# Kernel optimization log

Measured on AMD Instinct MI355X. Metric: run time of the kernel, lower is better.

## Reference

```python
import jax, jax.numpy as jnp
import numpy as np

N_NODES = 40000
N_EDGES = 640000
IN_DIM = 128
HID = 128
N_GRAPHS = 256
N_CLASSES = 1


def setup_inputs() -> dict:
    key = jax.random.key(0)
    ks = jax.random.split(key, 16)
    h = jax.random.normal(ks[0], (N_NODES, IN_DIM), dtype=jnp.float32)
    src = jax.random.randint(ks[1], (N_EDGES,), 0, N_NODES, dtype=jnp.int32)
    dst = jax.random.randint(ks[2], (N_EDGES,), 0, N_NODES, dtype=jnp.int32)
    graph_ids = jnp.sort(jax.random.randint(ks[3], (N_NODES,), 0, N_GRAPHS, dtype=jnp.int32))
    s = 1.0 / np.sqrt(HID)
    W1 = jax.random.normal(ks[4], (IN_DIM, HID), dtype=jnp.float32) * s
    b1 = jnp.zeros((HID,), jnp.float32)
    W2 = jax.random.normal(ks[5], (HID, HID), dtype=jnp.float32) * s
    b2 = jnp.zeros((HID,), jnp.float32)
    Wc1 = jax.random.normal(ks[6], (HID, HID), dtype=jnp.float32) * s
    bc1 = jnp.zeros((HID,), jnp.float32)
    Wc2 = jax.random.normal(ks[7], (HID, HID), dtype=jnp.float32) * s
    bc2 = jnp.zeros((HID,), jnp.float32)
    Wc3 = jax.random.normal(ks[8], (HID, N_CLASSES), dtype=jnp.float32) * s
    bc3 = jnp.zeros((N_CLASSES,), jnp.float32)
    return dict(h=h, src=src, dst=dst, graph_ids=graph_ids,
                W1=W1, b1=b1, W2=W2, b2=b2,
                Wc1=Wc1, bc1=bc1, Wc2=Wc2, bc2=bc2, Wc3=Wc3, bc3=bc3)


def _graph_conv(h, src, dst, W, b):
    # DGL GraphConv with norm='both': out = D_in^{-1/2} A D_out^{-1/2} h W + b
    ones = jnp.ones((src.shape[0],), h.dtype)
    deg_out = jax.ops.segment_sum(ones, src, num_segments=N_NODES)
    deg_in = jax.ops.segment_sum(ones, dst, num_segments=N_NODES)
    norm_s = jnp.clip(deg_out, 1.0, None) ** -0.5  # [N]
    norm_d = jnp.clip(deg_in, 1.0, None) ** -0.5
    # mult weight first (in_dim >= out_dim path in DGL); math identical either way
    hw = (h * norm_s[:, None]) @ W                  # [N, HID]
    agg = jax.ops.segment_sum(hw[src], dst, num_segments=N_NODES)  # gather-scatter
    return agg * norm_d[:, None] + b


def reference(h, src, dst, graph_ids, W1, b1, W2, b2, Wc1, bc1, Wc2, bc2, Wc3, bc3):
    h1 = jax.nn.relu(_graph_conv(h, src, dst, W1, b1))
    h1 = jax.nn.relu(_graph_conv(h1, src, dst, W2, b2))
    # dgl.mean_nodes: per-graph mean over nodes
    sums = jax.ops.segment_sum(h1, graph_ids, num_segments=N_GRAPHS)      # [G, HID]
    counts = jax.ops.segment_sum(jnp.ones((N_NODES,), h1.dtype), graph_ids,
                                 num_segments=N_GRAPHS)
    hg = sums / jnp.maximum(counts, 1.0)[:, None]
    out = jax.nn.relu(hg @ Wc1 + bc1)
    out = jax.nn.relu(out @ Wc2 + bc2)
    return out @ Wc3 + bc3
```

## Files before the change

kernel.cpp:

```cpp
#include <hip/hip_runtime.h>

#define HID 128
#define CAP 64
#define HBLK 160
#define PERIOD 21

typedef unsigned int uint;
typedef unsigned short ushort;

typedef __attribute__((ext_vector_type(8))) short short8;
typedef __attribute__((ext_vector_type(4))) float floatx4;

static __device__ __forceinline__ ushort f2bf(float f) {
    uint u = __float_as_uint(f);
    u += 0x7fffu + ((u >> 16) & 1u);
    return (ushort)(u >> 16);
}
static __device__ __forceinline__ float bf2f(ushort v) {
    return __uint_as_float(((uint)v) << 16);
}

__global__ void gc_wpack(const float* __restrict__ W1, const float* __restrict__ W2,
                         uint4* __restrict__ wpk) {
    int which = blockIdx.x;
    const float* W = which ? W2 : W1;
    uint4* o = wpk + (size_t)which * 2048;
    for (int i = threadIdx.x; i < 2048; i += 256) {
        int lane = i & 63;
        int kc = (i >> 6) & 3;
        int nt = i >> 8;
        int n = nt * 16 + (lane & 15);
        int k0 = kc * 32 + (lane >> 4) * 8;
        uint p[4];
        #pragma unroll
        for (int j = 0; j < 4; ++j) {
            ushort a = f2bf(W[(size_t)(k0 + 2 * j) * HID + n]);
            ushort b = f2bf(W[(size_t)(k0 + 2 * j + 1) * HID + n]);
            p[j] = (uint)a | ((uint)b << 16);
        }
        uint4 v; v.x = p[0]; v.y = p[1]; v.z = p[2]; v.w = p[3];
        o[i] = v;
    }
}

__global__ void gc_build_mm(const int* __restrict__ src, const int* __restrict__ dst,
                            int* __restrict__ cnt_in, ushort* __restrict__ slot,
                            uint* __restrict__ pblock,
                            const float* __restrict__ X, const uint4* __restrict__ wpk,
                            ushort* __restrict__ hw, int n_edges, int n_nodes) {
    __shared__ uint hb4[10000];
    int b = blockIdx.x;
    int r = b % PERIOD, q = b / PERIOD;
    int t = threadIdx.x;

    if (r < 16) {
        int bi = q * 16 + r;
        if (bi >= 2500) return;
        int e = bi * 256 + t;
        if (e < n_edges) {
            int s = src[e], d = dst[e];
            int pos = atomicAdd(&cnt_in[d], 1);
            if (pos < CAP) slot[(size_t)d * CAP + pos] = (ushort)s;
        }
    } else if (r == 16) {
        int hq = q;
        if (hq >= HBLK) return;
        for (int i = t; i < 10000; i += 256) hb4[i] = 0u;
        __syncthreads();
        int per = (n_edges + HBLK - 1) / HBLK;
        int e0 = hq * per, e1 = min(e0 + per, n_edges);
        for (int e = e0 + t; e < e1; e += 256) {
            int s = src[e];
            atomicAdd(&hb4[s >> 2], 1u << ((s & 3) * 8));
        }
        __syncthreads();
        uint* o = pblock + (size_t)hq * 10000;
        for (int i = t; i < 10000; i += 256) o[i] = hb4[i];
    } else {
        int mb = q * 4 + (r - 17);
        if (mb >= 625) return;
        int wave = (mb * 256 + t) >> 6;
        int lane = t & 63;
        int tiles = n_nodes >> 4;
        if (wave >= tiles) return;
        int m = lane & 15, quad = lane >> 4;
        int node = wave * 16 + m;
        const float* xrow = X + (size_t)node * HID;

        floatx4 acc[8];
        #pragma unroll
        for (int nt = 0; nt < 8; ++nt) acc[nt] = (floatx4){0.f, 0.f, 0.f, 0.f};

        #pragma unroll
        for (int kc = 0; kc < 4; ++kc) {
            const float4 xa = *reinterpret_cast<const float4*>(xrow + kc * 32 + quad * 8);
            const float4 xb = *reinterpret_cast<const float4*>(xrow + kc * 32 + quad * 8 + 4);
            uint4 xu;
            xu.x = (uint)f2bf(xa.x) | ((uint)f2bf(xa.y) << 16);
            xu.y = (uint)f2bf(xa.z) | ((uint)f2bf(xa.w) << 16);
            xu.z = (uint)f2bf(xb.x) | ((uint)f2bf(xb.y) << 16);
            xu.w = (uint)f2bf(xb.z) | ((uint)f2bf(xb.w) << 16);
            short8 xf = *reinterpret_cast<short8*>(&xu);
            #pragma unroll
            for (int nt = 0; nt < 8; ++nt) {
                uint4 wu = wpk[(size_t)(nt * 4 + kc) * 64 + lane];
                short8 wf = *reinterpret_cast<short8*>(&wu);
                acc[nt] = __builtin_amdgcn_mfma_f32_16x16x32_bf16(wf, xf, acc[nt], 0, 0, 0);
            }
        }
        #pragma unroll
        for (int nt = 0; nt < 8; ++nt) {
            uint2 v;
            v.x = (uint)f2bf(acc[nt][0]) | ((uint)f2bf(acc[nt][1]) << 16);
            v.y = (uint)f2bf(acc[nt][2]) | ((uint)f2bf(acc[nt][3]) << 16);
            *reinterpret_cast<uint2*>(hw + (size_t)node * HID + nt * 16 + quad * 4) = v;
        }
    }
}

__global__ void gc_reduce(const uint* __restrict__ pblock, float* __restrict__ norm_s,
                          int n_nodes) {
    int i = blockIdx.x * blockDim.x + threadIdx.x;
    if (i >= 10000) return;
    uint a0 = 0, a1 = 0, a2 = 0, a3 = 0;
    for (int b = 0; b < HBLK; ++b) {
        uint v = pblock[(size_t)b * 10000 + i];
        a0 += v & 0xffu;
        a1 += (v >> 8) & 0xffu;
        a2 += (v >> 16) & 0xffu;
        a3 += v >> 24;
    }
    float4 o;
    o.x = rsqrtf(fmaxf((float)a0, 1.0f));
    o.y = rsqrtf(fmaxf((float)a1, 1.0f));
    o.z = rsqrtf(fmaxf((float)a2, 1.0f));
    o.w = rsqrtf(fmaxf((float)a3, 1.0f));
    *reinterpret_cast<float4*>(norm_s + i * 4) = o;
}

__global__ void gc_gather_mm(const ushort* __restrict__ HW, const int* __restrict__ cnt_in,
                             const float* __restrict__ norm_s, const ushort* __restrict__ slot,
                             const float* __restrict__ b, const uint4* __restrict__ wpk2,
                             ushort* __restrict__ hw2, int n_nodes) {
    __shared__ ushort tile[16 * HID];
    int tid = threadIdx.x;
    int ts = tid >> 4;
    int l16 = tid & 15;
    int node = blockIdx.x * 16 + ts;
    int q = l16 << 3;

    int ci = cnt_in[node];
    int cnt = min(ci, CAP);
    const ushort* row = slot + (size_t)node * CAP;
    float a[8];
    #pragma unroll
    for (int j = 0; j < 8; ++j) a[j] = 0.0f;

    auto accum = [&](uint4 u, float ns) {
        a[0] = fmaf(ns, __uint_as_float(u.x << 16), a[0]);
        a[1] = fmaf(ns, __uint_as_float(u.x & 0xffff0000u), a[1]);
        a[2] = fmaf(ns, __uint_as_float(u.y << 16), a[2]);
        a[3] = fmaf(ns, __uint_as_float(u.y & 0xffff0000u), a[3]);
        a[4] = fmaf(ns, __uint_as_float(u.z << 16), a[4]);
        a[5] = fmaf(ns, __uint_as_float(u.z & 0xffff0000u), a[5]);
        a[6] = fmaf(ns, __uint_as_float(u.w << 16), a[6]);
        a[7] = fmaf(ns, __uint_as_float(u.w & 0xffff0000u), a[7]);
    };

    int e = 0;
    for (; e + 3 < cnt; e += 4) {
        int s0 = row[e], s1 = row[e + 1], s2 = row[e + 2], s3 = row[e + 3];
        uint4 u0 = *reinterpret_cast<const uint4*>(HW + (size_t)s0 * HID + q);
        uint4 u1 = *reinterpret_cast<const uint4*>(HW + (size_t)s1 * HID + q);
        uint4 u2 = *reinterpret_cast<const uint4*>(HW + (size_t)s2 * HID + q);
        uint4 u3 = *reinterpret_cast<const uint4*>(HW + (size_t)s3 * HID + q);
        float n0 = norm_s[s0], n1 = norm_s[s1], n2 = norm_s[s2], n3 = norm_s[s3];
        accum(u0, n0); accum(u1, n1); accum(u2, n2); accum(u3, n3);
    }
    for (; e < cnt; ++e) {
        int s0 = row[e];
        uint4 u0 = *reinterpret_cast<const uint4*>(HW + (size_t)s0 * HID + q);
        accum(u0, norm_s[s0]);
    }

    float nd = rsqrtf(fmaxf((float)ci, 1.0f));
    const float4 bv0 = *reinterpret_cast<const float4*>(b + q);
    const float4 bv1 = *reinterpret_cast<const float4*>(b + q + 4);
    float r[8];
    r[0] = fmaxf(a[0] * nd + bv0.x, 0.0f);
    r[1] = fmaxf(a[1] * nd + bv0.y, 0.0f);
    r[2] = fmaxf(a[2] * nd + bv0.z, 0.0f);
    r[3] = fmaxf(a[3] * nd + bv0.w, 0.0f);
    r[4] = fmaxf(a[4] * nd + bv1.x, 0.0f);
    r[5] = fmaxf(a[5] * nd + bv1.y, 0.0f);
    r[6] = fmaxf(a[6] * nd + bv1.z, 0.0f);
    r[7] = fmaxf(a[7] * nd + bv1.w, 0.0f);
    uint4 v;
    v.x = (uint)f2bf(r[0]) | ((uint)f2bf(r[1]) << 16);
    v.y = (uint)f2bf(r[2]) | ((uint)f2bf(r[3]) << 16);
    v.z = (uint)f2bf(r[4]) | ((uint)f2bf(r[5]) << 16);
    v.w = (uint)f2bf(r[6]) | ((uint)f2bf(r[7]) << 16);
    *reinterpret_cast<uint4*>(&tile[ts * HID + ((l16 ^ ts) << 3)]) = v;
    __syncthreads();

    int wv = tid >> 6;
    int lane = tid & 63;
    int m = lane & 15, quad = lane >> 4;
    int onode = blockIdx.x * 16 + m;

    floatx4 acc0 = (floatx4){0.f, 0.f, 0.f, 0.f};
    floatx4 acc1 = (floatx4){0.f, 0.f, 0.f, 0.f};
    int nt0 = wv * 2, nt1 = wv * 2 + 1;
    #pragma unroll
    for (int kc = 0; kc < 4; ++kc) {
        int cc = (kc * 4 + quad) ^ m;
        uint4 xu = *reinterpret_cast<const uint4*>(&tile[m * HID + (cc << 3)]);
        short8 xf = *reinterpret_cast<short8*>(&xu);
        uint4 w0 = wpk2[(size_t)(nt0 * 4 + kc) * 64 + lane];
        uint4 w1 = wpk2[(size_t)(nt1 * 4 + kc) * 64 + lane];
        short8 wf0 = *reinterpret_cast<short8*>(&w0);
        short8 wf1 = *reinterpret_cast<short8*>(&w1);
        acc0 = __builtin_amdgcn_mfma_f32_16x16x32_bf16(wf0, xf, acc0, 0, 0, 0);
        acc1 = __builtin_amdgcn_mfma_f32_16x16x32_bf16(wf1, xf, acc1, 0, 0, 0);
    }
    float ns = norm_s[onode];
    {
        uint2 o0, o1;
        o0.x = (uint)f2bf(acc0[0] * ns) | ((uint)f2bf(acc0[1] * ns) << 16);
        o0.y = (uint)f2bf(acc0[2] * ns) | ((uint)f2bf(acc0[3] * ns) << 16);
        o1.x = (uint)f2bf(acc1[0] * ns) | ((uint)f2bf(acc1[1] * ns) << 16);
        o1.y = (uint)f2bf(acc1[2] * ns) | ((uint)f2bf(acc1[3] * ns) << 16);
        *reinterpret_cast<uint2*>(hw2 + (size_t)onode * HID + nt0 * 16 + quad * 4) = o0;
        *reinterpret_cast<uint2*>(hw2 + (size_t)onode * HID + nt1 * 16 + quad * 4) = o1;
    }
}

__global__ void gc_gather_pool(const ushort* __restrict__ HW, const int* __restrict__ cnt_in,
                               const ushort* __restrict__ slot, const int* __restrict__ gid,
                               const float* __restrict__ b, float* __restrict__ part2,
                               int n_nodes) {
    __shared__ float tile[16 * HID];
    __shared__ int sgid[16];
    int tid = threadIdx.x;
    int ts = tid >> 4;
    int l16 = tid & 15;
    int node = blockIdx.x * 16 + ts;
    int q = l16 << 3;
    int ci = cnt_in[node];
    int cnt = min(ci, CAP);
    const ushort* row = slot + (size_t)node * CAP;
    if (l16 == 0) sgid[ts] = gid[node];
    float a[8];
    #pragma unroll
    for (int j = 0; j < 8; ++j) a[j] = 0.0f;

    auto accum = [&](uint4 u) {
        a[0] += __uint_as_float(u.x << 16);
        a[1] += __uint_as_float(u.x & 0xffff0000u);
        a[2] += __uint_as_float(u.y << 16);
        a[3] += __uint_as_float(u.y & 0xffff0000u);
        a[4] += __uint_as_float(u.z << 16);
        a[5] += __uint_as_float(u.z & 0xffff0000u);
        a[6] += __uint_as_float(u.w << 16);
        a[7] += __uint_as_float(u.w & 0xffff0000u);
    };

    int e = 0;
    for (; e + 3 < cnt; e += 4) {
        int s0 = row[e], s1 = row[e + 1], s2 = row[e + 2], s3 = row[e + 3];
        uint4 u0 = *reinterpret_cast<const uint4*>(HW + (size_t)s0 * HID + q);
        uint4 u1 = *reinterpret_cast<const uint4*>(HW + (size_t)s1 * HID + q);
        uint4 u2 = *reinterpret_cast<const uint4*>(HW + (size_t)s2 * HID + q);
        uint4 u3 = *reinterpret_cast<const uint4*>(HW + (size_t)s3 * HID + q);
        accum(u0); accum(u1); accum(u2); accum(u3);
    }
    for (; e < cnt; ++e) {
        uint4 u0 = *reinterpret_cast<const uint4*>(HW + (size_t)row[e] * HID + q);
        accum(u0);
    }

    float nd = rsqrtf(fmaxf((float)ci, 1.0f));
    const float4 bv0 = *reinterpret_cast<const float4*>(b + q);
    const float4 bv1 = *reinterpret_cast<const float4*>(b + q + 4);
    float* tr = tile + ts * HID + q;
    tr[0] = fmaxf(a[0] * nd + bv0.x, 0.0f);
    tr[1] = fmaxf(a[1] * nd + bv0.y, 0.0f);
    tr[2] = fmaxf(a[2] * nd + bv0.z, 0.0f);
    tr[3] = fmaxf(a[3] * nd + bv0.w, 0.0f);
    tr[4] = fmaxf(a[4] * nd + bv1.x, 0.0f);
    tr[5] = fmaxf(a[5] * nd + bv1.y, 0.0f);
    tr[6] = fmaxf(a[6] * nd + bv1.z, 0.0f);
    tr[7] = fmaxf(a[7] * nd + bv1.w, 0.0f);
    __syncthreads();

    int c = tid & 127;
    int which = tid >> 7;
    int g0 = sgid[0];
    float s = 0.0f;
    #pragma unroll
    for (int k = 0; k < 16; ++k) {
        bool mine = (sgid[k] == g0) == (which == 0);
        s += mine ? tile[k * HID + c] : 0.0f;
    }
    part2[((size_t)blockIdx.x * 2 + which) * HID + c] = s;
}

__global__ void gc_mlp(const float* __restrict__ part2, const int* __restrict__ gid,
                       int n_nodes,
                       const float* __restrict__ Wc1, const float* __restrict__ bc1,
                       const float* __restrict__ Wc2, const float* __restrict__ bc2,
                       const float* __restrict__ Wc3, const float* __restrict__ bc3,
                       float* __restrict__ out) {
    int g = blockIdx.x;
    int c = threadIdx.x;
    int beg, end;
    {
        int lo = 0, hi = n_nodes;
        while (lo < hi) { int mid = (lo + hi) >> 1; if (gid[mid] < g) lo = mid + 1; else hi = mid; }
        beg = lo;
        lo = beg; hi = n_nodes;
        while (lo < hi) { int mid = (lo + hi) >> 1; if (gid[mid] < g + 1) lo = mid + 1; else hi = mid; }
        end = lo;
    }
    float s = 0.0f;
    int b_lo = beg >> 4, b_hi = (end - 1) >> 4;
    for (int bb = b_lo; bb <= b_hi; ++bb) {
        int g0 = gid[bb * 16];
        if (g0 == g)     s += part2[((size_t)bb * 2 + 0) * HID + c];
        if (g0 == g - 1) s += part2[((size_t)bb * 2 + 1) * HID + c];
    }
    float inv = 1.0f / fmaxf((float)(end - beg), 1.0f);
    __shared__ float x[HID];
    __shared__ float y[HID];
    __shared__ float red[HID];
    x[c] = s * inv;
    __syncthreads();
    float a = bc1[c];
    for (int k = 0; k < HID; ++k) a += x[k] * Wc1[(size_t)k * HID + c];
    y[c] = fmaxf(a, 0.0f);
    __syncthreads();
    float a2 = bc2[c];
    for (int k = 0; k < HID; ++k) a2 += y[k] * Wc2[(size_t)k * HID + c];
    float z = fmaxf(a2, 0.0f);
    red[c] = z * Wc3[c];
    __syncthreads();
    for (int sr = 64; sr > 0; sr >>= 1) {
        if (c < sr) red[c] += red[c + sr];
        __syncthreads();
    }
    if (c == 0) out[g] = red[0] + bc3[0];
}

extern "C" void kernel_launch(void* const* d_in, const int* in_sizes, int n_in,
                              void* d_out, int out_size, void* d_ws, size_t ws_size,
                              hipStream_t stream) {
    const float* h    = (const float*)d_in[0];
    const int*   src  = (const int*)d_in[1];
    const int*   dst  = (const int*)d_in[2];
    const int*   gid  = (const int*)d_in[3];
    const float* W1   = (const float*)d_in[4];
    const float* b1   = (const float*)d_in[5];
    const float* W2   = (const float*)d_in[6];
    const float* b2   = (const float*)d_in[7];
    const float* Wc1  = (const float*)d_in[8];
    const float* bc1  = (const float*)d_in[9];
    const float* Wc2  = (const float*)d_in[10];
    const float* bc2  = (const float*)d_in[11];
    const float* Wc3  = (const float*)d_in[12];
    const float* bc3  = (const float*)d_in[13];
    float* out = (float*)d_out;

    const int n_nodes  = in_sizes[0] / HID;
    const int n_edges  = in_sizes[1];
    const int n_graphs = 256;

    char* wsb = (char*)d_ws;
    size_t off = 0;
    auto alloc = [&](size_t bytes) {
        void* p = wsb + off;
        off += (bytes + 15) & ~(size_t)15;
        return p;
    };

    float*  norm_s  = (float*)alloc((size_t)n_nodes * 4);
    int*    cnt_in  = (int*)alloc((size_t)n_nodes * 4);
    ushort* slot    = (ushort*)alloc((size_t)n_nodes * CAP * 2);
    uint*   pblock  = (uint*)alloc((size_t)HBLK * 10000 * 4);
    float*  part2   = (float*)alloc((size_t)(n_nodes / 16) * 2 * HID * 4);
    uint4*  wpk     = (uint4*)alloc((size_t)2 * 2048 * 16);
    ushort* hw      = (ushort*)alloc((size_t)n_nodes * HID * 2);
    ushort* hw2     = (ushort*)alloc((size_t)n_nodes * HID * 2);

    hipMemsetAsync(cnt_in, 0, (size_t)n_nodes * sizeof(int), stream);

    gc_wpack<<<2, 256, 0, stream>>>(W1, W2, wpk);

    gc_build_mm<<<PERIOD * 160, 256, 0, stream>>>(src, dst, cnt_in, slot, pblock,
                                                  h, wpk, hw, n_edges, n_nodes);
    gc_reduce<<<(10000 + 255) / 256, 256, 0, stream>>>(pblock, norm_s, n_nodes);

    const int ga_grid = n_nodes / 16;

    gc_gather_mm<<<ga_grid, 256, 0, stream>>>(hw, cnt_in, norm_s, slot, b1,
                                              wpk + 2048, hw2, n_nodes);
    gc_gather_pool<<<ga_grid, 256, 0, stream>>>(hw2, cnt_in, slot, gid, b2,
                                                part2, n_nodes);
    gc_mlp<<<n_graphs, HID, 0, stream>>>(part2, gid, n_nodes,
                                         Wc1, bc1, Wc2, bc2, Wc3, bc3, out);
}
```

Baseline: 209.5 us.

## Build in-edge slot lists via block histograms and prefix ranks instead of global atomics

Replaces the per-edge global atomicAdd on cnt_in with LDS per-block histograms of dst that also record each edge's local rank. A reduce pass then turns the per-block histograms into exclusive offsets and writes cnt_in, and a new fill kernel places each source in its slot. This removes contended global atomics and the memset, at the cost of an extra kernel launch, an extra 6.4MB partial-histogram buffer and a byte rank array. Slot order now becomes deterministic by edge order. The 8-bit per-block counters assume fewer than 256 same-destination edges per 4000-edge block.

```diff
diff --git a/kernel.cpp b/kernel.cpp
--- a/kernel.cpp
+++ b/kernel.cpp
@@ -3,10 +3,11 @@
 #define HID 128
 #define CAP 64
 #define HBLK 160
-#define PERIOD 21
+#define PERIOD 6
 
 typedef unsigned int uint;
 typedef unsigned short ushort;
+typedef unsigned char uchar;
 
 typedef __attribute__((ext_vector_type(8))) short short8;
 typedef __attribute__((ext_vector_type(4))) float floatx4;
@@ -15,9 +16,6 @@
     uint u = __float_as_uint(f);
     u += 0x7fffu + ((u >> 16) & 1u);
     return (ushort)(u >> 16);
-}
-static __device__ __forceinline__ float bf2f(ushort v) {
-    return __uint_as_float(((uint)v) << 16);
 }
 
 __global__ void gc_wpack(const float* __restrict__ W1, const float* __restrict__ W2,
@@ -43,41 +41,38 @@
     }
 }
 
-__global__ void gc_build_mm(const int* __restrict__ src, const int* __restrict__ dst,
-                            int* __restrict__ cnt_in, ushort* __restrict__ slot,
-                            uint* __restrict__ pblock,
-                            const float* __restrict__ X, const uint4* __restrict__ wpk,
-                            ushort* __restrict__ hw, int n_edges, int n_nodes) {
+__global__ void gc_hist_mm(const int* __restrict__ src, const int* __restrict__ dst,
+                           uint* __restrict__ pblockS, uint* __restrict__ pblockD,
+                           uchar* __restrict__ rank8,
+                           const float* __restrict__ X, const uint4* __restrict__ wpk,
+                           ushort* __restrict__ hw, int n_edges, int n_nodes) {
     __shared__ uint hb4[10000];
     int b = blockIdx.x;
     int r = b % PERIOD, q = b / PERIOD;
     int t = threadIdx.x;
 
-    if (r < 16) {
-        int bi = q * 16 + r;
-        if (bi >= 2500) return;
-        int e = bi * 256 + t;
-        if (e < n_edges) {
-            int s = src[e], d = dst[e];
-            int pos = atomicAdd(&cnt_in[d], 1);
-            if (pos < CAP) slot[(size_t)d * CAP + pos] = (ushort)s;
-        }
-    } else if (r == 16) {
-        int hq = q;
-        if (hq >= HBLK) return;
+    if (r < 2) {
+        if (q >= HBLK) return;
         for (int i = t; i < 10000; i += 256) hb4[i] = 0u;
         __syncthreads();
-        int per = (n_edges + HBLK - 1) / HBLK;
-        int e0 = hq * per, e1 = min(e0 + per, n_edges);
-        for (int e = e0 + t; e < e1; e += 256) {
-            int s = src[e];
-            atomicAdd(&hb4[s >> 2], 1u << ((s & 3) * 8));
+        int e0 = q * 4000, e1 = min(e0 + 4000, n_edges);
+        if (r == 0) {
+            for (int e = e0 + t; e < e1; e += 256) {
+                int s = src[e];
+                atomicAdd(&hb4[s >> 2], 1u << ((s & 3) * 8));
+            }
+        } else {
+            for (int e = e0 + t; e < e1; e += 256) {
+                int d = dst[e];
+                uint old = atomicAdd(&hb4[d >> 2], 1u << ((d & 3) * 8));
+                rank8[e] = (uchar)((old >> ((d & 3) * 8)) & 0xffu);
+            }
         }
         __syncthreads();
-        uint* o = pblock + (size_t)hq * 10000;
+        uint* o = (r == 0 ? pblockS : pblockD) + (size_t)q * 10000;
         for (int i = t; i < 10000; i += 256) o[i] = hb4[i];
     } else {
-        int mb = q * 4 + (r - 17);
+        int mb = q * 4 + (r - 2);
         if (mb >= 625) return;
         int wave = (mb * 256 + t) >> 6;
         int lane = t & 63;
@@ -118,24 +113,43 @@
     }
 }
 
-__global__ void gc_reduce(const uint* __restrict__ pblock, float* __restrict__ norm_s,
+__global__ void gc_reduce(const uint* __restrict__ pblockS, uint* __restrict__ pblockD,
+                          float* __restrict__ norm_s, int* __restrict__ cnt_in,
                           int n_nodes) {
     int i = blockIdx.x * blockDim.x + threadIdx.x;
     if (i >= 10000) return;
-    uint a0 = 0, a1 = 0, a2 = 0, a3 = 0;
+    uint s0 = 0, s1 = 0, s2 = 0, s3 = 0;
+    uint r0 = 0, r1 = 0, r2 = 0, r3 = 0;
     for (int b = 0; b < HBLK; ++b) {
-        uint v = pblock[(size_t)b * 10000 + i];
-        a0 += v & 0xffu;
-        a1 += (v >> 8) & 0xffu;
-        a2 += (v >> 16) & 0xffu;
-        a3 += v >> 24;
+        uint vS = pblockS[(size_t)b * 10000 + i];
+        s0 += vS & 0xffu; s1 += (vS >> 8) & 0xffu;
+        s2 += (vS >> 16) & 0xffu; s3 += vS >> 24;
+        size_t idx = (size_t)b * 10000 + i;
+        uint vD = pblockD[idx];
+        pblockD[idx] = r0 | (r1 << 8) | (r2 << 16) | (r3 << 24);
+        r0 += vD & 0xffu; r1 += (vD >> 8) & 0xffu;
+        r2 += (vD >> 16) & 0xffu; r3 += vD >> 24;
     }
     float4 o;
-    o.x = rsqrtf(fmaxf((float)a0, 1.0f));
-    o.y = rsqrtf(fmaxf((float)a1, 1.0f));
-    o.z = rsqrtf(fmaxf((float)a2, 1.0f));
-    o.w = rsqrtf(fmaxf((float)a3, 1.0f));
+    o.x = rsqrtf(fmaxf((float)s0, 1.0f));
+    o.y = rsqrtf(fmaxf((float)s1, 1.0f));
+    o.z = rsqrtf(fmaxf((float)s2, 1.0f));
+    o.w = rsqrtf(fmaxf((float)s3, 1.0f));
     *reinterpret_cast<float4*>(norm_s + i * 4) = o;
+    int4 c; c.x = (int)r0; c.y = (int)r1; c.z = (int)r2; c.w = (int)r3;
+    *reinterpret_cast<int4*>(cnt_in + i * 4) = c;
+}
+
+__global__ void gc_fill(const int* __restrict__ src, const int* __restrict__ dst,
+                        const uchar* __restrict__ rank8, const uint* __restrict__ pblockD,
+                        ushort* __restrict__ slot, int n_edges) {
+    int e = blockIdx.x * blockDim.x + threadIdx.x;
+    if (e >= n_edges) return;
+    int s = src[e], d = dst[e];
+    int b = e / 4000;
+    uint w = pblockD[(size_t)b * 10000 + (d >> 2)];
+    int pos = (int)((w >> ((d & 3) * 8)) & 0xffu) + (int)rank8[e];
+    if (pos < CAP) slot[(size_t)d * CAP + pos] = (ushort)s;
 }
 
 __global__ void gc_gather_mm(const ushort* __restrict__ HW, const int* __restrict__ cnt_in,
@@ -385,19 +399,22 @@
     float*  norm_s  = (float*)alloc((size_t)n_nodes * 4);
     int*    cnt_in  = (int*)alloc((size_t)n_nodes * 4);
     ushort* slot    = (ushort*)alloc((size_t)n_nodes * CAP * 2);
-    uint*   pblock  = (uint*)alloc((size_t)HBLK * 10000 * 4);
+    uint*   pblockS = (uint*)alloc((size_t)HBLK * 10000 * 4);
+    uint*   pblockD = (uint*)alloc((size_t)HBLK * 10000 * 4);
+    uchar*  rank8   = (uchar*)alloc((size_t)n_edges);
     float*  part2   = (float*)alloc((size_t)(n_nodes / 16) * 2 * HID * 4);
     uint4*  wpk     = (uint4*)alloc((size_t)2 * 2048 * 16);
     ushort* hw      = (ushort*)alloc((size_t)n_nodes * HID * 2);
     ushort* hw2     = (ushort*)alloc((size_t)n_nodes * HID * 2);
 
-    hipMemsetAsync(cnt_in, 0, (size_t)n_nodes * sizeof(int), stream);
-
     gc_wpack<<<2, 256, 0, stream>>>(W1, W2, wpk);
 
-    gc_build_mm<<<PERIOD * 160, 256, 0, stream>>>(src, dst, cnt_in, slot, pblock,
+    gc_hist_mm<<<PERIOD * HBLK, 256, 0, stream>>>(src, dst, pblockS, pblockD, rank8,
                                                   h, wpk, hw, n_edges, n_nodes);
-    gc_reduce<<<(10000 + 255) / 256, 256, 0, stream>>>(pblock, norm_s, n_nodes);
+    gc_reduce<<<(10000 + 255) / 256, 256, 0, stream>>>(pblockS, pblockD,
+                                                       norm_s, cnt_in, n_nodes);
+    gc_fill<<<(n_edges + 255) / 256, 256, 0, stream>>>(src, dst, rank8, pblockD,
+                                                       slot, n_edges);
 
     const int ga_grid = n_nodes / 16;
 
```

Result: slower. 218.7 us (+4.4%).
